# Kernel optimization log

Hardware: AMD Instinct MI355X
Metric: run time of the kernel (lower is better)

Reference implementation:

```python
import jax, jax.numpy as jnp
import numpy as np

D_MODEL = 1024
NUM_HEADS = 16
D_HEAD = D_MODEL // NUM_HEADS
MAX_SEQ_LEN = 2048
THETA = 10000.0
BATCH = 2
SEQ = 2048


def _rope_tables():
    # inv_freq over even dims; emb interleaves each freq twice: [f0,f0,f1,f1,...]
    inv_freq = 1.0 / (THETA ** (jnp.arange(0, D_HEAD, 2, dtype=jnp.float32) / D_HEAD))
    t = jnp.arange(MAX_SEQ_LEN, dtype=jnp.float32)
    freqs = jnp.einsum('i,j->ij', t, inv_freq)  # [S, d_head/2]
    emb = jnp.stack((freqs, freqs), axis=-1).reshape(MAX_SEQ_LEN, D_HEAD)
    return jnp.cos(emb), jnp.sin(emb)


def _rotate_half(x):
    # pairwise interleaved rotation: (x0,x1,x2,x3,...) -> (-x1,x0,-x3,x2,...)
    xr = x.reshape(x.shape[:-1] + (D_HEAD // 2, 2))
    x1, x2 = xr[..., 0], xr[..., 1]
    return jnp.stack((-x2, x1), axis=-1).reshape(x.shape)


def setup_inputs() -> dict:
    key = jax.random.key(0)
    ks = jax.random.split(key, 5)
    std = np.sqrt(2.0 / (D_MODEL + D_MODEL)).astype(np.float32)
    return {
        'in_features': jax.random.normal(ks[0], (BATCH, SEQ, D_MODEL), dtype=jnp.float32),
        'token_positions': jnp.arange(SEQ, dtype=jnp.int64) if jax.config.jax_enable_x64 else jnp.arange(SEQ, dtype=jnp.int32),
        'wq': jax.random.normal(ks[1], (D_MODEL, D_MODEL), dtype=jnp.float32) * std,
        'wk': jax.random.normal(ks[2], (D_MODEL, D_MODEL), dtype=jnp.float32) * std,
        'wv': jax.random.normal(ks[3], (D_MODEL, D_MODEL), dtype=jnp.float32) * std,
        'wo': jax.random.normal(ks[4], (D_MODEL, D_MODEL), dtype=jnp.float32) * std,
    }


def reference(in_features, token_positions, wq, wk, wv, wo):
    b, s, _ = in_features.shape
    cos_tab, sin_tab = _rope_tables()
    cos = cos_tab[token_positions]  # [s, d_head]
    sin = sin_tab[token_positions]

    def split_heads(t):  # [b, s, d_model] -> [b, h, s, d_head]
        return t.reshape(b, s, NUM_HEADS, D_HEAD).transpose(0, 2, 1, 3)

    q = split_heads(jnp.einsum('bsd,ed->bse', in_features, wq))
    k = split_heads(jnp.einsum('bsd,ed->bse', in_features, wk))
    v = split_heads(jnp.einsum('bsd,ed->bse', in_features, wv))

    q = q * cos + _rotate_half(q) * sin
    k = k * cos + _rotate_half(k) * sin

    scale = 1.0 / np.sqrt(D_HEAD).astype(np.float32)
    scores = jnp.einsum('bhqd,bhkd->bhqk', q, k) * scale  # [b,h,s,s]
    causal = jnp.tril(jnp.ones((s, s), dtype=bool))
    scores = jnp.where(causal, scores, -jnp.inf)
    weights = jax.nn.softmax(scores, axis=-1)
    out = jnp.einsum('bhqk,bhkd->bhqd', weights, v)
    out = out.transpose(0, 2, 1, 3).reshape(b, s, D_MODEL)
    return jnp.einsum('bsd,ed->bse', out, wo)
```

## Files before the change

### kernel.cpp

```cpp
#include <hip/hip_runtime.h>


typedef __attribute__((ext_vector_type(8))) short bf16x8;
typedef __attribute__((ext_vector_type(4))) float f32x4;

__device__ __forceinline__ short f2bf(float f) {
  unsigned u = __float_as_uint(f);
  unsigned r = (u + 0x7fffu + ((u >> 16) & 1u)) >> 16;
  return (short)(r & 0xFFFFu);
}

__device__ __forceinline__ unsigned pk2(float a, float b) {
  return __builtin_amdgcn_perm(__float_as_uint(b) + 0x8000u,
                               __float_as_uint(a) + 0x8000u, 0x07060302u);
}

__device__ __forceinline__ void async16(const void* g, void* l) {
  __builtin_amdgcn_global_load_lds(
      (const __attribute__((address_space(1))) void*)g,
      (__attribute__((address_space(3))) void*)l, 16, 0, 0);
}

__device__ __forceinline__ void cstore(short* C, size_t i, float v) { C[i] = f2bf(v); }
__device__ __forceinline__ void cstore(float* C, size_t i, float v) { C[i] = v; }

__global__ void cast_all(const float4* __restrict__ X,
                         const float4* __restrict__ w0, const float4* __restrict__ w1,
                         const float4* __restrict__ w2, const float4* __restrict__ w3,
                         short* __restrict__ Xb, short* __restrict__ Wb) {
  int t = blockIdx.x * 256 + threadIdx.x;
  const float4* s;
  short4* d;
  if (t < (1 << 20)) {
    s = X + t; d = (short4*)Xb + t;
  } else {
    int u = t - (1 << 20);
    int which = u >> 18;
    s = ((which == 0) ? w0 : (which == 1) ? w1 : (which == 2) ? w2 : w3) + (u & 0x3FFFF);
    d = (short4*)Wb + u;
  }
  float4 v = *s;
  *d = make_short4(f2bf(v.x), f2bf(v.y), f2bf(v.z), f2bf(v.w));
}

template <typename OUT, int MR, int NR, bool ROPE>
__device__ __forceinline__ void gemm_core(short* __restrict__ As, short* __restrict__ Bs,
                                          const short* __restrict__ A, const short* __restrict__ B,
                                          OUT* __restrict__ C, int bm, int bn, int ldc,
                                          const int* __restrict__ pos) {
  constexpr int BM = 32 * MR, BN = 32 * NR;
  const int tid  = threadIdx.x;
  const int lane = tid & 63, wave = tid >> 6;
  const int col  = lane & 15, quad = lane >> 4;
  const int wm = (wave & 1) * (16 * MR), wn = (wave >> 1) * (16 * NR);

  f32x4 acc[MR][NR];
#pragma unroll
  for (int i = 0; i < MR; i++)
#pragma unroll
    for (int j = 0; j < NR; j++) acc[i][j] = (f32x4){0.f, 0.f, 0.f, 0.f};

  auto stage = [&](int k0, int bu) {
#pragma unroll
    for (int c = tid; c < BM * 4; c += 256) {
      int r = c >> 2, cc = (c & 3) << 3;
      async16(A + (size_t)(bm + r) * 1024 + k0 + cc, As + bu * BM * 32 + c * 8);
    }
#pragma unroll
    for (int c = tid; c < BN * 4; c += 256) {
      int r = c >> 2, cc = (c & 3) << 3;
      async16(B + (size_t)(bn + r) * 1024 + k0 + cc, Bs + bu * BN * 32 + c * 8);
    }
  };

  stage(0, 0);
  for (int it = 0; it < 32; ++it) {
    __syncthreads();
    if (it < 31) stage((it + 1) * 32, (it + 1) & 1);
    const short* as = As + (it & 1) * BM * 32;
    const short* bs = Bs + (it & 1) * BN * 32;

    bf16x8 af[MR], bfr[NR];
#pragma unroll
    for (int i = 0; i < MR; i++)
      af[i] = *(const bf16x8*)(as + (wm + i * 16 + col) * 32 + quad * 8);
#pragma unroll
    for (int i = 0; i < NR; i++)
      bfr[i] = *(const bf16x8*)(bs + (wn + i * 16 + col) * 32 + quad * 8);
#pragma unroll
    for (int mi = 0; mi < MR; mi++)
#pragma unroll
      for (int ni = 0; ni < NR; ni++)
        acc[mi][ni] = __builtin_amdgcn_mfma_f32_16x16x32_bf16(af[mi], bfr[ni], acc[mi][ni], 0, 0, 0);
  }

  if (ROPE) {
    float invf_rev[NR];
#pragma unroll
    for (int ni = 0; ni < NR; ni++) {
      int pr = ((bn + wn + ni * 16 + col) & 63) >> 1;
      invf_rev[ni] = exp2f(-0.4152410118609203f * (float)pr) * 0.15915494309189535f;
    }
    const float sgn = (col & 1) ? 1.f : -1.f;
#pragma unroll
    for (int mi = 0; mi < MR; mi++) {
#pragma unroll
      for (int r = 0; r < 4; r++) {
        int row = bm + wm + mi * 16 + quad * 4 + r;
        float fp = (float)pos[row & 2047];
#pragma unroll
        for (int ni = 0; ni < NR; ni++) {
          float rev = fp * invf_rev[ni];
          rev -= floorf(rev);
          float sn = __builtin_amdgcn_sinf(rev);
          float cs = __builtin_amdgcn_cosf(rev);
          float x  = acc[mi][ni][r];
          float px = __shfl_xor(x, 1);
          acc[mi][ni][r] = fmaf(x, cs, sgn * px * sn);
        }
      }
    }
  }

#pragma unroll
  for (int mi = 0; mi < MR; mi++) {
#pragma unroll
    for (int r = 0; r < 4; r++) {
      size_t row = (size_t)(bm + wm + mi * 16 + quad * 4 + r);
#pragma unroll
      for (int ni = 0; ni < NR; ni++) {
        int cg = bn + wn + ni * 16 + col;
        cstore(C, row * ldc + cg, acc[mi][ni][r]);
      }
    }
  }
}

__global__ __launch_bounds__(256) void qkv_gemm(const short* __restrict__ Xb,
                                                const short* __restrict__ Wq,
                                                const short* __restrict__ Wk,
                                                const short* __restrict__ Wv,
                                                short* __restrict__ Qo,
                                                short* __restrict__ Ko,
                                                short* __restrict__ Vto,
                                                const int* __restrict__ pos) {
  __shared__ __align__(16) short sm[2 * 128 * 32 + 2 * 128 * 32];
  short* As = sm;
  short* Bs = sm + 2 * 128 * 32;
  const int z = blockIdx.z;
  if (z == 0)      gemm_core<short, 4, 4, true >(As, Bs, Xb, Wq, Qo, blockIdx.x * 128, blockIdx.y * 128, 1024, pos);
  else if (z == 1) gemm_core<short, 4, 4, true >(As, Bs, Xb, Wk, Ko, blockIdx.x * 128, blockIdx.y * 128, 1024, pos);
  else             gemm_core<short, 4, 4, false>(As, Bs, Wv, Xb, Vto, blockIdx.y * 128, blockIdx.x * 128, 4096, pos);
}

__global__ __launch_bounds__(256) void out_gemm(const short* __restrict__ Ctx,
                                                const short* __restrict__ Wo,
                                                float* __restrict__ C) {
  __shared__ __align__(16) short sm[2 * 64 * 32 + 2 * 128 * 32];
  gemm_core<float, 2, 4, false>(sm, sm + 2 * 64 * 32, Ctx, Wo, C,
                                blockIdx.x * 64, blockIdx.y * 128, 1024, nullptr);
}

__global__ __launch_bounds__(256) void flash_attn(const short* __restrict__ Q,
                                                  const short* __restrict__ K,
                                                  const short* __restrict__ Vt,
                                                  short* __restrict__ ctx) {
  const int y = blockIdx.y;
  const int qt = (y < 8) ? y : 23 - y;
  const int bh = blockIdx.x;
  const int b = bh >> 4, h = bh & 15;
  __shared__ __align__(16) short Ks[2][64 * 64];
  __shared__ __align__(16) short Vs[2][64 * 64];
  __shared__ __align__(16) short Ps[4][32 * 72];
  const int tid = threadIdx.x, lane = tid & 63, wave = tid >> 6;
  const int col = lane & 15, quad = lane >> 4;

  bf16x8 qf[2][2];
#pragma unroll
  for (int g = 0; g < 2; g++) {
    const size_t qrow = (size_t)(b * 2048 + qt * 128 + wave * 32 + g * 16 + col);
    qf[g][0] = *(const bf16x8*)(Q + qrow * 1024 + h * 64 + quad * 8);
    qf[g][1] = *(const bf16x8*)(Q + qrow * 1024 + h * 64 + 32 + quad * 8);
  }

  float l_i[2] = {0.f, 0.f};
  f32x4 o_acc[2][4];
#pragma unroll
  for (int g = 0; g < 2; g++)
#pragma unroll
    for (int i = 0; i < 4; i++) o_acc[g][i] = (f32x4){0.f, 0.f, 0.f, 0.f};

  auto stage = [&](int kt, int bu) {
#pragma unroll
    for (int i = 0; i < 2; i++) {
      int c = i * 256 + tid;
      int r = c >> 3;
      int g = ((c & 7) ^ (r & 7)) << 3;
      async16(K  + (size_t)(b * 2048 + kt * 64 + r) * 1024 + h * 64 + g, Ks[bu] + c * 8);
      async16(Vt + (size_t)(h * 64 + r) * 4096 + b * 2048 + kt * 64 + g, Vs[bu] + c * 8);
    }
  };

  const float C1 = 0.18033688011112042f;
  const float C2 = 17.31234049066756f;

  auto tile = [&](int kt, bool diag) {
    const short* ks = Ks[kt & 1];
    const short* vs = Vs[kt & 1];
    f32x4 s_acc[2][4];
#pragma unroll
    for (int nb = 0; nb < 4; nb++) {
      int row = nb * 16 + col;
      bf16x8 k0 = *(const bf16x8*)(ks + (row * 8 + (quad ^ (row & 7))) * 8);
      bf16x8 k1 = *(const bf16x8*)(ks + (row * 8 + ((quad + 4) ^ (row & 7))) * 8);
#pragma unroll
      for (int g = 0; g < 2; g++) {
        f32x4 z = (f32x4){0.f, 0.f, 0.f, 0.f};
        z = __builtin_amdgcn_mfma_f32_16x16x32_bf16(k0, qf[g][0], z, 0, 0, 0);
        z = __builtin_amdgcn_mfma_f32_16x16x32_bf16(k1, qf[g][1], z, 0, 0, 0);
        s_acc[g][nb] = z;
      }
    }
#pragma unroll
    for (int g = 0; g < 2; g++) {
#pragma unroll
      for (int nb = 0; nb < 4; nb++) {
        float p[4];
#pragma unroll
        for (int r = 0; r < 4; r++) {
          p[r] = exp2f(s_acc[g][nb][r] * C1 - C2);
          if (diag) {
            int key = kt * 64 + nb * 16 + quad * 4 + r;
            int qg  = qt * 128 + wave * 32 + g * 16 + col;
            if (key > qg) p[r] = 0.f;
          }
          l_i[g] += p[r];
        }
        *(uint2*)(&Ps[wave][(g * 16 + col) * 72 + nb * 16 + quad * 4]) =
            make_uint2(pk2(p[0], p[1]), pk2(p[2], p[3]));
      }
    }
    bf16x8 af[2][2];
#pragma unroll
    for (int g = 0; g < 2; g++) {
      af[g][0] = *(const bf16x8*)(&Ps[wave][(g * 16 + col) * 72 + quad * 8]);
      af[g][1] = *(const bf16x8*)(&Ps[wave][(g * 16 + col) * 72 + 32 + quad * 8]);
    }
#pragma unroll
    for (int nb = 0; nb < 4; nb++) {
      int row = nb * 16 + col;
      bf16x8 v0 = *(const bf16x8*)(vs + (row * 8 + (quad ^ (row & 7))) * 8);
      bf16x8 v1 = *(const bf16x8*)(vs + (row * 8 + ((quad + 4) ^ (row & 7))) * 8);
#pragma unroll
      for (int g = 0; g < 2; g++) {
        o_acc[g][nb] = __builtin_amdgcn_mfma_f32_16x16x32_bf16(af[g][0], v0, o_acc[g][nb], 0, 0, 0);
        o_acc[g][nb] = __builtin_amdgcn_mfma_f32_16x16x32_bf16(af[g][1], v1, o_acc[g][nb], 0, 0, 0);
      }
    }
  };

  const int last = 2 * qt + 1;
  stage(0, 0);
  for (int kt = 0; kt <= last; ++kt) {
    __syncthreads();
    if (kt < last) stage(kt + 1, (kt + 1) & 1);
    if (kt < 2 * qt)                   tile(kt, false);
    else if (wave >= 2 || kt == 2 * qt) tile(kt, true);
  }

#pragma unroll
  for (int g = 0; g < 2; g++) {
    l_i[g] += __shfl_xor(l_i[g], 16);
    l_i[g] += __shfl_xor(l_i[g], 32);
  }

#pragma unroll
  for (int g = 0; g < 2; g++) {
    float invl = 1.0f / l_i[g];
#pragma unroll
    for (int r = 0; r < 4; r++) {
      float inv = __shfl(invl, quad * 4 + r);
      size_t row = (size_t)(b * 2048 + qt * 128 + wave * 32 + g * 16 + quad * 4 + r);
#pragma unroll
      for (int nb = 0; nb < 4; nb++)
        ctx[row * 1024 + h * 64 + nb * 16 + col] = f2bf(o_acc[g][nb][r] * inv);
    }
  }
}

extern "C" void kernel_launch(void* const* d_in, const int* in_sizes, int n_in,
                              void* d_out, int out_size, void* d_ws, size_t ws_size,
                              hipStream_t stream) {
  const float* X  = (const float*)d_in[0];
  const int* pos  = (const int*)d_in[1];
  const float* wq = (const float*)d_in[2];
  const float* wk = (const float*)d_in[3];
  const float* wv = (const float*)d_in[4];
  const float* wo = (const float*)d_in[5];
  float* out = (float*)d_out;

  short* Xb  = (short*)d_ws;
  short* Wqb = Xb + (1 << 22);
  short* Wkb = Wqb + (1 << 20);
  short* Wvb = Wkb + (1 << 20);
  short* Wob = Wvb + (1 << 20);
  short* Qb  = Wob + (1 << 20);
  short* Kb  = Qb + (1 << 22);
  short* Vtb = Kb + (1 << 22);
  short* Ctx = Vtb + (1 << 22);

  cast_all<<<8192, 256, 0, stream>>>((const float4*)X, (const float4*)wq, (const float4*)wk,
                                     (const float4*)wv, (const float4*)wo, Xb, Wqb);
  qkv_gemm<<<dim3(32, 8, 3), 256, 0, stream>>>(Xb, Wqb, Wkb, Wvb, Qb, Kb, Vtb, pos);
  flash_attn<<<dim3(32, 16), 256, 0, stream>>>(Qb, Kb, Vtb, Ctx);
  out_gemm<<<dim3(64, 8), 256, 0, stream>>>(Ctx, Wob, out);
}
```

Baseline: 194.1 us.

## Drop LDS staging in flash attention, load K/V directly per wave with 64-row Q tiles

```diff
diff --git a/kernel.cpp b/kernel.cpp
--- a/kernel.cpp
+++ b/kernel.cpp
@@ -161,130 +161,94 @@
                                 blockIdx.x * 64, blockIdx.y * 128, 1024, nullptr);
 }
 
-__global__ __launch_bounds__(256) void flash_attn(const short* __restrict__ Q,
-                                                  const short* __restrict__ K,
-                                                  const short* __restrict__ Vt,
-                                                  short* __restrict__ ctx) {
+__global__ __launch_bounds__(256, 4) void flash_attn(const short* __restrict__ Q,
+                                                     const short* __restrict__ K,
+                                                     const short* __restrict__ Vt,
+                                                     short* __restrict__ ctx) {
   const int y = blockIdx.y;
-  const int qt = (y < 8) ? y : 23 - y;
+  const int qt = (y & 1) ? (31 - (y >> 1)) : (y >> 1);
   const int bh = blockIdx.x;
   const int b = bh >> 4, h = bh & 15;
-  __shared__ __align__(16) short Ks[2][64 * 64];
-  __shared__ __align__(16) short Vs[2][64 * 64];
-  __shared__ __align__(16) short Ps[4][32 * 72];
+  __shared__ __align__(16) short Ps[4][16 * 72];
   const int tid = threadIdx.x, lane = tid & 63, wave = tid >> 6;
   const int col = lane & 15, quad = lane >> 4;
 
-  bf16x8 qf[2][2];
-#pragma unroll
-  for (int g = 0; g < 2; g++) {
-    const size_t qrow = (size_t)(b * 2048 + qt * 128 + wave * 32 + g * 16 + col);
-    qf[g][0] = *(const bf16x8*)(Q + qrow * 1024 + h * 64 + quad * 8);
-    qf[g][1] = *(const bf16x8*)(Q + qrow * 1024 + h * 64 + 32 + quad * 8);
-  }
-
-  float l_i[2] = {0.f, 0.f};
-  f32x4 o_acc[2][4];
-#pragma unroll
-  for (int g = 0; g < 2; g++)
-#pragma unroll
-    for (int i = 0; i < 4; i++) o_acc[g][i] = (f32x4){0.f, 0.f, 0.f, 0.f};
-
-  auto stage = [&](int kt, int bu) {
-#pragma unroll
-    for (int i = 0; i < 2; i++) {
-      int c = i * 256 + tid;
-      int r = c >> 3;
-      int g = ((c & 7) ^ (r & 7)) << 3;
-      async16(K  + (size_t)(b * 2048 + kt * 64 + r) * 1024 + h * 64 + g, Ks[bu] + c * 8);
-      async16(Vt + (size_t)(h * 64 + r) * 4096 + b * 2048 + kt * 64 + g, Vs[bu] + c * 8);
-    }
-  };
+  const short* Kb = K  + (size_t)(b * 2048) * 1024 + h * 64;
+  const short* Vb = Vt + (size_t)(h * 64) * 4096 + b * 2048;
+
+  const size_t qrow = (size_t)(b * 2048 + qt * 64 + wave * 16 + col);
+  bf16x8 qf0 = *(const bf16x8*)(Q + qrow * 1024 + h * 64 + quad * 8);
+  bf16x8 qf1 = *(const bf16x8*)(Q + qrow * 1024 + h * 64 + 32 + quad * 8);
+
+  float l_i = 0.f;
+  f32x4 o_acc[4];
+#pragma unroll
+  for (int i = 0; i < 4; i++) o_acc[i] = (f32x4){0.f, 0.f, 0.f, 0.f};
 
   const float C1 = 0.18033688011112042f;
   const float C2 = 17.31234049066756f;
-
-  auto tile = [&](int kt, bool diag) {
-    const short* ks = Ks[kt & 1];
-    const short* vs = Vs[kt & 1];
-    f32x4 s_acc[2][4];
-#pragma unroll
-    for (int nb = 0; nb < 4; nb++) {
-      int row = nb * 16 + col;
-      bf16x8 k0 = *(const bf16x8*)(ks + (row * 8 + (quad ^ (row & 7))) * 8);
-      bf16x8 k1 = *(const bf16x8*)(ks + (row * 8 + ((quad + 4) ^ (row & 7))) * 8);
-#pragma unroll
-      for (int g = 0; g < 2; g++) {
-        f32x4 z = (f32x4){0.f, 0.f, 0.f, 0.f};
-        z = __builtin_amdgcn_mfma_f32_16x16x32_bf16(k0, qf[g][0], z, 0, 0, 0);
-        z = __builtin_amdgcn_mfma_f32_16x16x32_bf16(k1, qf[g][1], z, 0, 0, 0);
-        s_acc[g][nb] = z;
+  const int qg = qt * 64 + wave * 16 + col;
+
+  short* myPs = &Ps[wave][0];
+  const int pswr = col * 72;
+  const int psrd = col * 72 + quad * 8;
+
+  for (int kt = 0; kt <= qt; ++kt) {
+    const int kbase = kt * 64;
+    bf16x8 kf[4][2];
+#pragma unroll
+    for (int nb = 0; nb < 4; nb++) {
+      const short* kp = Kb + (size_t)(kbase + nb * 16 + col) * 1024 + quad * 8;
+      kf[nb][0] = *(const bf16x8*)(kp);
+      kf[nb][1] = *(const bf16x8*)(kp + 32);
+    }
+    f32x4 s_acc[4];
+#pragma unroll
+    for (int nb = 0; nb < 4; nb++) {
+      f32x4 z = (f32x4){0.f, 0.f, 0.f, 0.f};
+      z = __builtin_amdgcn_mfma_f32_16x16x32_bf16(kf[nb][0], qf0, z, 0, 0, 0);
+      z = __builtin_amdgcn_mfma_f32_16x16x32_bf16(kf[nb][1], qf1, z, 0, 0, 0);
+      s_acc[nb] = z;
+    }
+    bf16x8 vf[4][2];
+#pragma unroll
+    for (int nb = 0; nb < 4; nb++) {
+      const short* vp = Vb + (size_t)(nb * 16 + col) * 4096 + kbase + quad * 8;
+      vf[nb][0] = *(const bf16x8*)(vp);
+      vf[nb][1] = *(const bf16x8*)(vp + 32);
+    }
+    const bool diag = (kt == qt);
+#pragma unroll
+    for (int nb = 0; nb < 4; nb++) {
+      float p[4];
+#pragma unroll
+      for (int r = 0; r < 4; r++) {
+        p[r] = exp2f(s_acc[nb][r] * C1 - C2);
+        if (diag && (kbase + nb * 16 + quad * 4 + r) > qg) p[r] = 0.f;
+        l_i += p[r];
       }
-    }
-#pragma unroll
-    for (int g = 0; g < 2; g++) {
-#pragma unroll
-      for (int nb = 0; nb < 4; nb++) {
-        float p[4];
-#pragma unroll
-        for (int r = 0; r < 4; r++) {
-          p[r] = exp2f(s_acc[g][nb][r] * C1 - C2);
-          if (diag) {
-            int key = kt * 64 + nb * 16 + quad * 4 + r;
-            int qg  = qt * 128 + wave * 32 + g * 16 + col;
-            if (key > qg) p[r] = 0.f;
-          }
-          l_i[g] += p[r];
-        }
-        *(uint2*)(&Ps[wave][(g * 16 + col) * 72 + nb * 16 + quad * 4]) =
-            make_uint2(pk2(p[0], p[1]), pk2(p[2], p[3]));
-      }
-    }
-    bf16x8 af[2][2];
-#pragma unroll
-    for (int g = 0; g < 2; g++) {
-      af[g][0] = *(const bf16x8*)(&Ps[wave][(g * 16 + col) * 72 + quad * 8]);
-      af[g][1] = *(const bf16x8*)(&Ps[wave][(g * 16 + col) * 72 + 32 + quad * 8]);
-    }
-#pragma unroll
-    for (int nb = 0; nb < 4; nb++) {
-      int row = nb * 16 + col;
-      bf16x8 v0 = *(const bf16x8*)(vs + (row * 8 + (quad ^ (row & 7))) * 8);
-      bf16x8 v1 = *(const bf16x8*)(vs + (row * 8 + ((quad + 4) ^ (row & 7))) * 8);
-#pragma unroll
-      for (int g = 0; g < 2; g++) {
-        o_acc[g][nb] = __builtin_amdgcn_mfma_f32_16x16x32_bf16(af[g][0], v0, o_acc[g][nb], 0, 0, 0);
-        o_acc[g][nb] = __builtin_amdgcn_mfma_f32_16x16x32_bf16(af[g][1], v1, o_acc[g][nb], 0, 0, 0);
-      }
-    }
-  };
-
-  const int last = 2 * qt + 1;
-  stage(0, 0);
-  for (int kt = 0; kt <= last; ++kt) {
-    __syncthreads();
-    if (kt < last) stage(kt + 1, (kt + 1) & 1);
-    if (kt < 2 * qt)                   tile(kt, false);
-    else if (wave >= 2 || kt == 2 * qt) tile(kt, true);
-  }
-
-#pragma unroll
-  for (int g = 0; g < 2; g++) {
-    l_i[g] += __shfl_xor(l_i[g], 16);
-    l_i[g] += __shfl_xor(l_i[g], 32);
-  }
-
-#pragma unroll
-  for (int g = 0; g < 2; g++) {
-    float invl = 1.0f / l_i[g];
-#pragma unroll
-    for (int r = 0; r < 4; r++) {
-      float inv = __shfl(invl, quad * 4 + r);
-      size_t row = (size_t)(b * 2048 + qt * 128 + wave * 32 + g * 16 + quad * 4 + r);
-#pragma unroll
-      for (int nb = 0; nb < 4; nb++)
-        ctx[row * 1024 + h * 64 + nb * 16 + col] = f2bf(o_acc[g][nb][r] * inv);
-    }
+      *(uint2*)(myPs + pswr + nb * 16 + quad * 4) = make_uint2(pk2(p[0], p[1]), pk2(p[2], p[3]));
+    }
+    bf16x8 af0 = *(const bf16x8*)(myPs + psrd);
+    bf16x8 af1 = *(const bf16x8*)(myPs + psrd + 32);
+#pragma unroll
+    for (int nb = 0; nb < 4; nb++) {
+      o_acc[nb] = __builtin_amdgcn_mfma_f32_16x16x32_bf16(af0, vf[nb][0], o_acc[nb], 0, 0, 0);
+      o_acc[nb] = __builtin_amdgcn_mfma_f32_16x16x32_bf16(af1, vf[nb][1], o_acc[nb], 0, 0, 0);
+    }
+  }
+
+  l_i += __shfl_xor(l_i, 16);
+  l_i += __shfl_xor(l_i, 32);
+  float invl = 1.0f / l_i;
+
+#pragma unroll
+  for (int r = 0; r < 4; r++) {
+    float inv = __shfl(invl, quad * 4 + r);
+    size_t row = (size_t)(b * 2048 + qt * 64 + wave * 16 + quad * 4 + r);
+#pragma unroll
+    for (int nb = 0; nb < 4; nb++)
+      ctx[row * 1024 + h * 64 + nb * 16 + col] = f2bf(o_acc[nb][r] * inv);
   }
 }
 
@@ -312,6 +276,6 @@
   cast_all<<<8192, 256, 0, stream>>>((const float4*)X, (const float4*)wq, (const float4*)wk,
                                      (const float4*)wv, (const float4*)wo, Xb, Wqb);
   qkv_gemm<<<dim3(32, 8, 3), 256, 0, stream>>>(Xb, Wqb, Wkb, Wvb, Qb, Kb, Vtb, pos);
-  flash_attn<<<dim3(32, 16), 256, 0, stream>>>(Qb, Kb, Vtb, Ctx);
+  flash_attn<<<dim3(32, 32), 256, 0, stream>>>(Qb, Kb, Vtb, Ctx);
   out_gemm<<<dim3(64, 8), 256, 0, stream>>>(Ctx, Wob, out);
 }
```

Measured after the change: 318.7 us. +64.2%, slower.
